# Optimization experiments

Measured on AMD Instinct MI355X. Metric: run time of the kernel, lower is better.

The kernel has to match this reference:

```python
import jax, jax.numpy as jnp
from jax import lax
import numpy as np

T = 16  # decode_times
NEG_SLOPE = 0.01  # LeakyReLU default


def setup_inputs() -> dict:
    key = jax.random.key(0)
    ks = jax.random.split(key, 8)
    H = 256  # hidden_size
    C = 256  # input_size
    O = 2    # linear_output_size
    s = 1.0 / np.sqrt(H)
    return {
        "x": jax.random.normal(ks[0], (8, C, 40, 40), jnp.float32),
        "hx": jnp.zeros((12800, H), jnp.float32),
        "cx": jnp.zeros((12800, H), jnp.float32),
        "W_ih": jax.random.uniform(ks[1], (4 * H, C), jnp.float32, -s, s),
        "W_hh": jax.random.uniform(ks[2], (4 * H, H), jnp.float32, -s, s),
        "b_ih": jax.random.uniform(ks[3], (4 * H,), jnp.float32, -s, s),
        "b_hh": jax.random.uniform(ks[4], (4 * H,), jnp.float32, -s, s),
        "W_lin": jax.random.uniform(ks[5], (O, H), jnp.float32, -s, s),
        "b_lin": jax.random.uniform(ks[6], (O,), jnp.float32, -s, s),
    }


def reference(x, hx, cx, W_ih, W_hh, b_ih, b_hh, W_lin, b_lin):
    bs, c, h, w = x.shape
    # BSxCxHxW -> (BS*H*W, C): same flattening as permute(0,2,3,1).reshape(-1, C)
    xf = jnp.transpose(x, (0, 2, 3, 1)).reshape(-1, c)
    # Input projection is identical every step (same x fed each time)
    x_proj = xf @ W_ih.T + b_ih + b_hh  # [N, 4H]

    def step(carry, _):
        hx, cx = carry
        gates = x_proj + hx @ W_hh.T  # [N, 4H]
        i, f, g, o = jnp.split(gates, 4, axis=-1)  # torch LSTMCell gate order
        i = jax.nn.sigmoid(i)
        f = jax.nn.sigmoid(f)
        g = jnp.tanh(g)
        o = jax.nn.sigmoid(o)
        cx = f * cx + i * g
        hx = o * jnp.tanh(cx)
        return (hx, cx), hx

    _, outs = lax.scan(step, (hx, cx), None, length=T)  # [T, N, H]
    # Dropout(0.1) is identity in eval mode; LeakyReLU then Linear head
    y = jax.nn.leaky_relu(outs, NEG_SLOPE)
    y = jnp.einsum('tnh,oh->tno', y, W_lin) + b_lin  # [T, N, O]
    y = y.reshape(T, bs, h, w, -1)
    return jnp.transpose(y, (1, 2, 3, 0, 4))  # [BS, H, W, T, O]
```

## Files before the change

### kernel.cpp

```cpp
#include <hip/hip_runtime.h>
#include <stdint.h>
#include <stddef.h>

typedef _Float16 half_t;
typedef half_t half8  __attribute__((ext_vector_type(8)));
typedef half_t half4v __attribute__((ext_vector_type(4)));
typedef float  f32x4  __attribute__((ext_vector_type(4)));

__device__ __forceinline__ float fast_sigmoid(float x) {
    float e = __builtin_amdgcn_exp2f(-1.44269504f * x);
    return __builtin_amdgcn_rcpf(1.0f + e);
}
__device__ __forceinline__ float fast_tanh(float x) {
    float e = __builtin_amdgcn_exp2f(2.88539008f * x);
    return 1.0f - 2.0f * __builtin_amdgcn_rcpf(1.0f + e);
}

__global__ __launch_bounds__(64) void shuffle_w_kernel(
    const float* __restrict__ W, half_t* __restrict__ out)
{
    const int blk = blockIdx.x;
    const int T = blk >> 3, kt = blk & 7;
    const int l = threadIdx.x;
    const int w = (T & 15) >> 1, j = T & 1, g = T >> 4;
    const int v = g * 2 + j;
    const int col = T * 16 + (l & 15);
    const int k0 = kt * 32 + ((l >> 4) << 3);
    half8 vv;
#pragma unroll
    for (int e = 0; e < 8; ++e) vv[e] = (half_t)W[col * 256 + k0 + e];
    *reinterpret_cast<half8*>(
        out + ((size_t)((w * 8 + kt) * 8 + v) * 64 + l) * 8) = vv;
}

template <typename CoWork>
__device__ __forceinline__ void gemm_all(
    f32x4* acc, const half_t* __restrict__ lhx,
    const half_t* Ws, int w, int lm, int lg, int l, CoWork&& cowork)
{
    asm volatile("" : "+v"(Ws));
    const half_t* wb = Ws + (size_t)w * 32768 + l * 8;
#pragma unroll 1
    for (int kt = 0; kt < 8; ++kt) {
        const half_t* q0 = wb + kt * 4096;
        const half_t* q1 = q0 + 2048;
        half8 b[8];
#pragma unroll
        for (int v = 0; v < 4; ++v) {
            b[v]     = *reinterpret_cast<const half8*>(q0 + v * 512);
            b[4 + v] = *reinterpret_cast<const half8*>(q1 + v * 512);
        }
        half8 a[4];
#pragma unroll
        for (int mt = 0; mt < 4; ++mt) {
            const int p = mt * 16 + lm;
            const int k = (kt * 32 + lg * 8) ^ ((p & 7) << 4);
            a[mt] = *reinterpret_cast<const half8*>(&lhx[p * 256 + k]);
        }
#pragma unroll
        for (int v = 0; v < 8; ++v)
#pragma unroll
            for (int mt = 0; mt < 4; ++mt)
                acc[mt * 8 + v] = __builtin_amdgcn_mfma_f32_16x16x32_f16(
                    a[mt], b[v], acc[mt * 8 + v], 0, 0, 0);
        cowork(kt);
        __builtin_amdgcn_sched_barrier(0);
    }
}

__global__ __launch_bounds__(512)
void lstm_kernel(
    const float* __restrict__ x,
    const float* __restrict__ hx0,
    const float* __restrict__ cx0,
    const float* __restrict__ b_ih,
    const float* __restrict__ b_hh,
    const float* __restrict__ W_lin,
    const float* __restrict__ b_lin,
    const half_t* __restrict__ Wih_s,
    const half_t* __restrict__ Whh_s,
    float* __restrict__ out)
{
    __shared__ __align__(16) half_t lds_hx[64 * 256];
    __shared__ __align__(16) half_t lds_xp[8 * 32 * 64 * 4];

    const int tid = threadIdx.x;
    const int w  = tid >> 6;
    const int l  = tid & 63;
    const int lm = l & 15;
    const int lg = l >> 4;
    const int w2 = w * 2;

    const int row0 = blockIdx.x * 64;
    const int bb_  = row0 / 1600;
    const int p0   = row0 % 1600;

    {
        const float* xin = x + (size_t)bb_ * 409600 + p0;
        for (int it = 0; it < 32; ++it) {
            int idx = it * 512 + tid;
            int p = idx & 63, c = idx >> 6;
            lds_hx[p * 256 + (c ^ ((p & 7) << 4))] = (half_t)xin[c * 1600 + p];
        }
    }
    __syncthreads();

    f32x4 acc[32];
    auto nocw = [](int) {};

#pragma unroll
    for (int g = 0; g < 4; ++g)
#pragma unroll
        for (int j = 0; j < 2; ++j) {
            int col = (g * 16 + w2 + j) * 16 + lm;
            float bias = b_ih[col] + b_hh[col];
#pragma unroll
            for (int mt = 0; mt < 4; ++mt)
                acc[mt * 8 + g * 2 + j] = (f32x4){bias, bias, bias, bias};
        }
    gemm_all(acc, lds_hx, Wih_s, w, lm, lg, l, nocw);

#pragma unroll
    for (int f = 0; f < 32; ++f) {
        half4v xv;
#pragma unroll
        for (int r = 0; r < 4; ++r) xv[r] = (half_t)acc[f][r];
        *reinterpret_cast<half4v*>(&lds_xp[((w * 32 + f) * 64 + l) * 4]) = xv;
    }
    __syncthreads();

    {
        const float* hin = hx0 + (size_t)row0 * 256;
        for (int it = 0; it < 32; ++it) {
            int idx = it * 512 + tid;
            int c = idx & 255, p = idx >> 8;
            lds_hx[p * 256 + (c ^ ((p & 7) << 4))] = (half_t)hin[p * 256 + c];
        }
    }
    float cxr[32];
#pragma unroll
    for (int mt = 0; mt < 4; ++mt)
#pragma unroll
        for (int j = 0; j < 2; ++j)
#pragma unroll
            for (int r = 0; r < 4; ++r) {
                int p = mt * 16 + lg * 4 + r;
                int c = w * 32 + j * 16 + lm;
                cxr[(mt * 2 + j) * 4 + r] = cx0[(size_t)(row0 + p) * 256 + c];
            }
    const float blin0 = b_lin[0], blin1 = b_lin[1];
    const int ph = tid >> 3;
    const int ho = (tid >> 2) & 1;
    const int hq = tid & 3;
    __syncthreads();

#pragma unroll 1
    for (int t = 0; t < 16; ++t) {
        const float* wl = W_lin + ho * 256 + hq * 64;
        asm volatile("" : "+v"(wl));
        float hs = 0.0f;
        float4 hwv0, hwv1;
        if (t > 0) {
            hwv0 = *reinterpret_cast<const float4*>(wl + 0);
            hwv1 = *reinterpret_cast<const float4*>(wl + 4);
        }
        auto head_cw = [&](int wi) {
            if (t > 0) {
#pragma unroll
                for (int ii = 0; ii < 2; ++ii) {
                    int cb = wi * 2 + ii;
                    int c0 = hq * 64 + cb * 4;
                    half4v u = *reinterpret_cast<const half4v*>(
                        &lds_hx[ph * 256 + (c0 ^ ((ph & 7) << 4))]);
                    float4 wv = ii ? hwv1 : hwv0;
                    if (cb + 2 < 16) {
                        float4 nx = *reinterpret_cast<const float4*>(
                            wl + (cb + 2) * 4);
                        if (ii) hwv1 = nx; else hwv0 = nx;
                    }
                    float h0 = (float)u[0], h1 = (float)u[1];
                    float h2 = (float)u[2], h3 = (float)u[3];
                    hs += fmaxf(h0, 0.01f * h0) * wv.x;
                    hs += fmaxf(h1, 0.01f * h1) * wv.y;
                    hs += fmaxf(h2, 0.01f * h2) * wv.z;
                    hs += fmaxf(h3, 0.01f * h3) * wv.w;
                }
            }
        };

#pragma unroll
        for (int fc = 0; fc < 32; fc += 4) {
#pragma unroll
            for (int f = fc; f < fc + 4; ++f) {
                half4v u = *reinterpret_cast<const half4v*>(
                    &lds_xp[((w * 32 + f) * 64 + l) * 4]);
#pragma unroll
                for (int r = 0; r < 4; ++r) acc[f][r] = (float)u[r];
            }
            __builtin_amdgcn_sched_barrier(0);
        }

        gemm_all(acc, lds_hx, Whh_s, w, lm, lg, l, head_cw);
        if (t > 0) {
            hs += __shfl_xor(hs, 1);
            hs += __shfl_xor(hs, 2);
            if (hq == 0)
                out[((size_t)(row0 + ph) * 16 + (t - 1)) * 2 + ho] =
                    hs + (ho ? blin1 : blin0);
        }

        __syncthreads();

#pragma unroll
        for (int mt = 0; mt < 4; ++mt)
#pragma unroll
            for (int j = 0; j < 2; ++j)
#pragma unroll
                for (int r = 0; r < 4; ++r) {
                    const int ci = (mt * 2 + j) * 4 + r;
                    float iv = acc[mt * 8 + 0 + j][r];
                    float fv = acc[mt * 8 + 2 + j][r];
                    float gv = acc[mt * 8 + 4 + j][r];
                    float ov = acc[mt * 8 + 6 + j][r];
                    float cxn = fast_sigmoid(fv) * cxr[ci] +
                                fast_sigmoid(iv) * fast_tanh(gv);
                    cxr[ci] = cxn;
                    float h = fast_sigmoid(ov) * fast_tanh(cxn);
                    int p  = mt * 16 + lg * 4 + r;
                    int cc = w * 32 + j * 16 + lm;
                    lds_hx[p * 256 + (cc ^ ((p & 7) << 4))] = (half_t)h;
                }
        __syncthreads();
    }

    {
        const float* wl = W_lin + ho * 256 + hq * 64;
        asm volatile("" : "+v"(wl));
        float s = 0.0f;
#pragma unroll 2
        for (int cb = 0; cb < 16; ++cb) {
            int c0 = hq * 64 + cb * 4;
            half4v u = *reinterpret_cast<const half4v*>(
                &lds_hx[ph * 256 + (c0 ^ ((ph & 7) << 4))]);
            float4 wv = *reinterpret_cast<const float4*>(wl + cb * 4);
            float h0 = (float)u[0], h1 = (float)u[1];
            float h2 = (float)u[2], h3 = (float)u[3];
            s += fmaxf(h0, 0.01f * h0) * wv.x;
            s += fmaxf(h1, 0.01f * h1) * wv.y;
            s += fmaxf(h2, 0.01f * h2) * wv.z;
            s += fmaxf(h3, 0.01f * h3) * wv.w;
        }
        s += __shfl_xor(s, 1);
        s += __shfl_xor(s, 2);
        if (hq == 0)
            out[((size_t)(row0 + ph) * 16 + 15) * 2 + ho] =
                s + (ho ? blin1 : blin0);
    }
}

extern "C" void kernel_launch(void* const* d_in, const int* in_sizes, int n_in,
                              void* d_out, int out_size, void* d_ws, size_t ws_size,
                              hipStream_t stream)
{
    const float* x    = (const float*)d_in[0];
    const float* hx   = (const float*)d_in[1];
    const float* cx   = (const float*)d_in[2];
    const float* Wih  = (const float*)d_in[3];
    const float* Whh  = (const float*)d_in[4];
    const float* bih  = (const float*)d_in[5];
    const float* bhh  = (const float*)d_in[6];
    const float* Wlin = (const float*)d_in[7];
    const float* blin = (const float*)d_in[8];
    float* out = (float*)d_out;

    half_t* wih_s = (half_t*)d_ws;
    half_t* whh_s = wih_s + 1024 * 256;

    shuffle_w_kernel<<<512, 64, 0, stream>>>(Wih, wih_s);
    shuffle_w_kernel<<<512, 64, 0, stream>>>(Whh, whh_s);
    lstm_kernel<<<200, 512, 0, stream>>>(x, hx, cx, bih, bhh, Wlin, blin,
                                         wih_s, whh_s, out);
}
```

Before: 239.1 us.

## Retile LSTM kernel to 32-row blocks of 4 waves, 64 gate columns each

Halves rows per workgroup from 64 to 32 and uses 4 waves of 256 threads, each wave now owning 64 gate columns instead of 32. The weight shuffle layout is changed to match, and the GEMM loop is split into two half-passes of 8 B-fragments each. The grid doubles to 400 blocks to fill more CUs, and launch bounds request 2 blocks per CU. Each weight fragment is now reused across only 2 row tiles instead of 4, so weight traffic from L2 per row doubles in exchange for better CU coverage.

```diff
diff --git a/kernel.cpp b/kernel.cpp
--- a/kernel.cpp
+++ b/kernel.cpp
@@ -22,15 +22,15 @@
     const int blk = blockIdx.x;
     const int T = blk >> 3, kt = blk & 7;
     const int l = threadIdx.x;
-    const int w = (T & 15) >> 1, j = T & 1, g = T >> 4;
-    const int v = g * 2 + j;
+    const int g = T >> 4, wj = T & 15, w = wj >> 2, j = wj & 3;
+    const int v = g * 4 + j;
     const int col = T * 16 + (l & 15);
     const int k0 = kt * 32 + ((l >> 4) << 3);
     half8 vv;
 #pragma unroll
     for (int e = 0; e < 8; ++e) vv[e] = (half_t)W[col * 256 + k0 + e];
     *reinterpret_cast<half8*>(
-        out + ((size_t)((w * 8 + kt) * 8 + v) * 64 + l) * 8) = vv;
+        out + (((size_t)(w * 8 + kt) * 16 + v) * 64 + l) * 8) = vv;
 }
 
 template <typename CoWork>
@@ -39,36 +39,49 @@
     const half_t* Ws, int w, int lm, int lg, int l, CoWork&& cowork)
 {
     asm volatile("" : "+v"(Ws));
-    const half_t* wb = Ws + (size_t)w * 32768 + l * 8;
+    const half_t* wb = Ws + (size_t)w * 65536 + l * 8;
 #pragma unroll 1
     for (int kt = 0; kt < 8; ++kt) {
-        const half_t* q0 = wb + kt * 4096;
-        const half_t* q1 = q0 + 2048;
-        half8 b[8];
-#pragma unroll
-        for (int v = 0; v < 4; ++v) {
-            b[v]     = *reinterpret_cast<const half8*>(q0 + v * 512);
-            b[4 + v] = *reinterpret_cast<const half8*>(q1 + v * 512);
-        }
-        half8 a[4];
-#pragma unroll
-        for (int mt = 0; mt < 4; ++mt) {
+        const half_t* q = wb + kt * 8192;
+        half8 a[2];
+#pragma unroll
+        for (int mt = 0; mt < 2; ++mt) {
             const int p = mt * 16 + lm;
             const int k = (kt * 32 + lg * 8) ^ ((p & 7) << 4);
             a[mt] = *reinterpret_cast<const half8*>(&lhx[p * 256 + k]);
         }
-#pragma unroll
-        for (int v = 0; v < 8; ++v)
-#pragma unroll
-            for (int mt = 0; mt < 4; ++mt)
-                acc[mt * 8 + v] = __builtin_amdgcn_mfma_f32_16x16x32_f16(
-                    a[mt], b[v], acc[mt * 8 + v], 0, 0, 0);
-        cowork(kt);
-        __builtin_amdgcn_sched_barrier(0);
-    }
-}
-
-__global__ __launch_bounds__(512)
+        {
+            half8 b[8];
+#pragma unroll
+            for (int vv = 0; vv < 8; ++vv)
+                b[vv] = *reinterpret_cast<const half8*>(q + vv * 512);
+#pragma unroll
+            for (int vv = 0; vv < 8; ++vv)
+#pragma unroll
+                for (int mt = 0; mt < 2; ++mt)
+                    acc[mt * 16 + vv] = __builtin_amdgcn_mfma_f32_16x16x32_f16(
+                        a[mt], b[vv], acc[mt * 16 + vv], 0, 0, 0);
+            cowork(kt * 2);
+            __builtin_amdgcn_sched_barrier(0);
+        }
+        {
+            half8 b[8];
+#pragma unroll
+            for (int vv = 0; vv < 8; ++vv)
+                b[vv] = *reinterpret_cast<const half8*>(q + 4096 + vv * 512);
+#pragma unroll
+            for (int vv = 0; vv < 8; ++vv)
+#pragma unroll
+                for (int mt = 0; mt < 2; ++mt)
+                    acc[mt * 16 + 8 + vv] = __builtin_amdgcn_mfma_f32_16x16x32_f16(
+                        a[mt], b[vv], acc[mt * 16 + 8 + vv], 0, 0, 0);
+            cowork(kt * 2 + 1);
+            __builtin_amdgcn_sched_barrier(0);
+        }
+    }
+}
+
+__global__ __launch_bounds__(256, 2)
 void lstm_kernel(
     const float* __restrict__ x,
     const float* __restrict__ hx0,
@@ -81,25 +94,24 @@
     const half_t* __restrict__ Whh_s,
     float* __restrict__ out)
 {
-    __shared__ __align__(16) half_t lds_hx[64 * 256];
-    __shared__ __align__(16) half_t lds_xp[8 * 32 * 64 * 4];
+    __shared__ __align__(16) half_t lds_hx[32 * 256];
+    __shared__ __align__(16) half_t lds_xp[4 * 32 * 64 * 4];
 
     const int tid = threadIdx.x;
     const int w  = tid >> 6;
     const int l  = tid & 63;
     const int lm = l & 15;
     const int lg = l >> 4;
-    const int w2 = w * 2;
-
-    const int row0 = blockIdx.x * 64;
+
+    const int row0 = blockIdx.x * 32;
     const int bb_  = row0 / 1600;
     const int p0   = row0 % 1600;
 
     {
         const float* xin = x + (size_t)bb_ * 409600 + p0;
         for (int it = 0; it < 32; ++it) {
-            int idx = it * 512 + tid;
-            int p = idx & 63, c = idx >> 6;
+            int idx = it * 256 + tid;
+            int p = idx & 31, c = idx >> 5;
             lds_hx[p * 256 + (c ^ ((p & 7) << 4))] = (half_t)xin[c * 1600 + p];
         }
     }
@@ -111,12 +123,12 @@
 #pragma unroll
     for (int g = 0; g < 4; ++g)
 #pragma unroll
-        for (int j = 0; j < 2; ++j) {
-            int col = (g * 16 + w2 + j) * 16 + lm;
+        for (int j = 0; j < 4; ++j) {
+            int col = (g * 16 + w * 4 + j) * 16 + lm;
             float bias = b_ih[col] + b_hh[col];
 #pragma unroll
-            for (int mt = 0; mt < 4; ++mt)
-                acc[mt * 8 + g * 2 + j] = (f32x4){bias, bias, bias, bias};
+            for (int mt = 0; mt < 2; ++mt)
+                acc[mt * 16 + g * 4 + j] = (f32x4){bias, bias, bias, bias};
         }
     gemm_all(acc, lds_hx, Wih_s, w, lm, lg, l, nocw);
 
@@ -132,21 +144,21 @@
     {
         const float* hin = hx0 + (size_t)row0 * 256;
         for (int it = 0; it < 32; ++it) {
-            int idx = it * 512 + tid;
+            int idx = it * 256 + tid;
             int c = idx & 255, p = idx >> 8;
             lds_hx[p * 256 + (c ^ ((p & 7) << 4))] = (half_t)hin[p * 256 + c];
         }
     }
     float cxr[32];
 #pragma unroll
-    for (int mt = 0; mt < 4; ++mt)
-#pragma unroll
-        for (int j = 0; j < 2; ++j)
+    for (int mt = 0; mt < 2; ++mt)
+#pragma unroll
+        for (int j = 0; j < 4; ++j)
 #pragma unroll
             for (int r = 0; r < 4; ++r) {
                 int p = mt * 16 + lg * 4 + r;
-                int c = w * 32 + j * 16 + lm;
-                cxr[(mt * 2 + j) * 4 + r] = cx0[(size_t)(row0 + p) * 256 + c];
+                int c = w * 64 + j * 16 + lm;
+                cxr[(mt * 4 + j) * 4 + r] = cx0[(size_t)(row0 + p) * 256 + c];
             }
     const float blin0 = b_lin[0], blin1 = b_lin[1];
     const int ph = tid >> 3;
@@ -159,32 +171,22 @@
         const float* wl = W_lin + ho * 256 + hq * 64;
         asm volatile("" : "+v"(wl));
         float hs = 0.0f;
-        float4 hwv0, hwv1;
-        if (t > 0) {
-            hwv0 = *reinterpret_cast<const float4*>(wl + 0);
-            hwv1 = *reinterpret_cast<const float4*>(wl + 4);
-        }
+        float4 hwv;
+        if (t > 0) hwv = *reinterpret_cast<const float4*>(wl);
         auto head_cw = [&](int wi) {
             if (t > 0) {
-#pragma unroll
-                for (int ii = 0; ii < 2; ++ii) {
-                    int cb = wi * 2 + ii;
-                    int c0 = hq * 64 + cb * 4;
-                    half4v u = *reinterpret_cast<const half4v*>(
-                        &lds_hx[ph * 256 + (c0 ^ ((ph & 7) << 4))]);
-                    float4 wv = ii ? hwv1 : hwv0;
-                    if (cb + 2 < 16) {
-                        float4 nx = *reinterpret_cast<const float4*>(
-                            wl + (cb + 2) * 4);
-                        if (ii) hwv1 = nx; else hwv0 = nx;
-                    }
-                    float h0 = (float)u[0], h1 = (float)u[1];
-                    float h2 = (float)u[2], h3 = (float)u[3];
-                    hs += fmaxf(h0, 0.01f * h0) * wv.x;
-                    hs += fmaxf(h1, 0.01f * h1) * wv.y;
-                    hs += fmaxf(h2, 0.01f * h2) * wv.z;
-                    hs += fmaxf(h3, 0.01f * h3) * wv.w;
-                }
+                int c0 = hq * 64 + wi * 4;
+                half4v u = *reinterpret_cast<const half4v*>(
+                    &lds_hx[ph * 256 + (c0 ^ ((ph & 7) << 4))]);
+                float4 wv = hwv;
+                if (wi < 15)
+                    hwv = *reinterpret_cast<const float4*>(wl + (wi + 1) * 4);
+                float h0 = (float)u[0], h1 = (float)u[1];
+                float h2 = (float)u[2], h3 = (float)u[3];
+                hs += fmaxf(h0, 0.01f * h0) * wv.x;
+                hs += fmaxf(h1, 0.01f * h1) * wv.y;
+                hs += fmaxf(h2, 0.01f * h2) * wv.z;
+                hs += fmaxf(h3, 0.01f * h3) * wv.w;
             }
         };
 
@@ -212,22 +214,22 @@
         __syncthreads();
 
 #pragma unroll
-        for (int mt = 0; mt < 4; ++mt)
-#pragma unroll
-            for (int j = 0; j < 2; ++j)
+        for (int mt = 0; mt < 2; ++mt)
+#pragma unroll
+            for (int j = 0; j < 4; ++j)
 #pragma unroll
                 for (int r = 0; r < 4; ++r) {
-                    const int ci = (mt * 2 + j) * 4 + r;
-                    float iv = acc[mt * 8 + 0 + j][r];
-                    float fv = acc[mt * 8 + 2 + j][r];
-                    float gv = acc[mt * 8 + 4 + j][r];
-                    float ov = acc[mt * 8 + 6 + j][r];
+                    const int ci = (mt * 4 + j) * 4 + r;
+                    float iv = acc[mt * 16 + 0 + j][r];
+                    float fv = acc[mt * 16 + 4 + j][r];
+                    float gv = acc[mt * 16 + 8 + j][r];
+                    float ov = acc[mt * 16 + 12 + j][r];
                     float cxn = fast_sigmoid(fv) * cxr[ci] +
                                 fast_sigmoid(iv) * fast_tanh(gv);
                     cxr[ci] = cxn;
                     float h = fast_sigmoid(ov) * fast_tanh(cxn);
                     int p  = mt * 16 + lg * 4 + r;
-                    int cc = w * 32 + j * 16 + lm;
+                    int cc = w * 64 + j * 16 + lm;
                     lds_hx[p * 256 + (cc ^ ((p & 7) << 4))] = (half_t)h;
                 }
         __syncthreads();
@@ -278,6 +280,6 @@
 
     shuffle_w_kernel<<<512, 64, 0, stream>>>(Wih, wih_s);
     shuffle_w_kernel<<<512, 64, 0, stream>>>(Whh, whh_s);
-    lstm_kernel<<<200, 512, 0, stream>>>(x, hx, cx, bih, bhh, Wlin, blin,
+    lstm_kernel<<<400, 256, 0, stream>>>(x, hx, cx, bih, bhh, Wlin, blin,
                                          wih_s, whh_s, out);
 }
```

Result: slower. 287.7 us (+20.3%).
